# Kernel tuning notes

Hardware: AMD Instinct MI355X
Metric: run time of the kernel (lower is better)

## Reference

```python
import jax, jax.numpy as jnp
import numpy as np

EMB = 1024
HEADS = 16
HEAD_DIM = EMB // HEADS
N = 16384


def setup_inputs() -> dict:
    key = jax.random.key(0)
    ks = jax.random.split(key, 9)
    s = 1.0 / np.sqrt(EMB)
    return {
        "src": jax.random.normal(ks[0], (N, EMB), dtype=jnp.float32),
        "Wq": jax.random.normal(ks[1], (EMB, EMB), dtype=jnp.float32) * s,
        "bq": jax.random.normal(ks[2], (EMB,), dtype=jnp.float32) * s,
        "Wk": jax.random.normal(ks[3], (EMB, EMB), dtype=jnp.float32) * s,
        "bk": jax.random.normal(ks[4], (EMB,), dtype=jnp.float32) * s,
        "Wv": jax.random.normal(ks[5], (EMB, EMB), dtype=jnp.float32) * s,
        "bv": jax.random.normal(ks[6], (EMB,), dtype=jnp.float32) * s,
        "Wo": jax.random.normal(ks[7], (EMB, EMB), dtype=jnp.float32) * s,
        "bo": jax.random.normal(ks[8], (EMB,), dtype=jnp.float32) * s,
    }


def reference(src, Wq, bq, Wk, bk, Wv, bv, Wo, bo):
    # nn.Linear: y = x @ W^T + b  (W is [out, in])
    q = src @ Wq.T + bq          # [N, E]
    k = src @ Wk.T + bk
    v = src @ Wv.T + bv
    q = q.reshape(-1, HEADS, HEAD_DIM)   # [N, H, D]
    k = k.reshape(-1, HEADS, HEAD_DIM)
    v = v.reshape(-1, HEADS, HEAD_DIM)
    # NOTE: attention is across heads within each token: scores [N, H, H]
    scale = 1.0 / jnp.sqrt(jnp.float32(HEAD_DIM))
    scores = jnp.einsum('nhd,ngd->nhg', q, k) * scale   # [N, H, H]
    attn = jax.nn.softmax(scores, axis=-1)
    out = jnp.einsum('nhg,ngd->nhd', attn, v)            # [N, H, D]
    out = out.reshape(-1, EMB)
    out = out @ Wo.T + bo                                 # [N, E]
    return out.reshape(-1, HEADS, HEAD_DIM)               # [N, H, D]
```

## Files before the change

### kernel.cpp

```cpp
#include <hip/hip_runtime.h>
#include <stdint.h>
#include <stddef.h>

#define EMB 1024
#define NTOK 16384

typedef __attribute__((ext_vector_type(8))) short short8;
typedef __attribute__((ext_vector_type(4))) float floatx4;

__device__ __forceinline__ unsigned short f2bf(float f) {
    union { float f; unsigned int u; } v; v.f = f;
    unsigned int u = v.u;
    unsigned int r = (u + 0x7fffu + ((u >> 16) & 1u)) >> 16;
    return (unsigned short)r;
}
__device__ __forceinline__ float bf2f(unsigned short s) {
    union { unsigned int u; float f; } v; v.u = ((unsigned int)s) << 16;
    return v.f;
}

__device__ __forceinline__ void gload16(const void* g, void* l) {
    __builtin_amdgcn_global_load_lds(
        (const __attribute__((address_space(1))) void*)g,
        (__attribute__((address_space(3))) void*)l, 16, 0, 0);
}

__global__ void cvt_kernel(const float* __restrict__ in,
                           unsigned short* __restrict__ out, int n4) {
    int idx = blockIdx.x * blockDim.x + threadIdx.x;
    int stride = gridDim.x * blockDim.x;
    for (int i = idx; i < n4; i += stride) {
        float4 f = reinterpret_cast<const float4*>(in)[i];
        ushort4 o;
        o.x = f2bf(f.x); o.y = f2bf(f.y); o.z = f2bf(f.z); o.w = f2bf(f.w);
        reinterpret_cast<ushort4*>(out)[i] = o;
    }
}

__global__ void cvt4_kernel(const float* __restrict__ s0, const float* __restrict__ s1,
                            const float* __restrict__ s2, const float* __restrict__ s3,
                            unsigned short* __restrict__ out) {
    int idx = blockIdx.x * blockDim.x + threadIdx.x;
    const int total = 4 << 18;
    int stride = gridDim.x * blockDim.x;
    for (int i = idx; i < total; i += stride) {
        int w = i >> 18, r = i & ((1 << 18) - 1);
        const float* s = (w == 0) ? s0 : (w == 1) ? s1 : (w == 2) ? s2 : s3;
        float4 f = reinterpret_cast<const float4*>(s)[r];
        ushort4 o;
        o.x = f2bf(f.x); o.y = f2bf(f.y); o.z = f2bf(f.z); o.w = f2bf(f.w);
        reinterpret_cast<ushort4*>(out)[i] = o;
    }
}

__global__ void bias_cat_kernel(const float* __restrict__ b0,
                                const float* __restrict__ b1,
                                const float* __restrict__ b2,
                                float* __restrict__ out) {
    int i = blockIdx.x * blockDim.x + threadIdx.x;
    float v = (i < 1024) ? b0[i] : (i < 2048 ? b1[i - 1024] : b2[i - 2048]);
    out[i] = v;
}

__device__ __forceinline__ void store_val(float* C, size_t idx, float v) { C[idx] = v; }
__device__ __forceinline__ void store_val(unsigned short* C, size_t idx, float v) { C[idx] = f2bf(v); }

template<typename OUT_T>
__global__ __launch_bounds__(512, 2)
void gemm256(const unsigned short* __restrict__ A,
             const unsigned short* __restrict__ B,
             const float* __restrict__ bias,
             OUT_T* __restrict__ C,
             int K, int Nc, int grid_m)
{
    __shared__ unsigned short lds[65536];

    const int bid = blockIdx.x;
    const int cpx = gridDim.x >> 3;
    const int wg  = (bid & 7) * cpx + (bid >> 3);
    const int m0 = (wg % grid_m) * 256;
    const int n0 = (wg / grid_m) * 256;

    const int tid  = threadIdx.x;
    const int lane = tid & 63;
    const int wid  = tid >> 6;
    const int wm = (wid >> 2) * 128;
    const int wn = (wid & 3) * 64;
    const int rr = lane & 15;
    const int klo = (((lane >> 4) ^ ((rr >> 1) & 3)) << 3);

    const unsigned short* pA[2];
    const unsigned short* pB[2];
    int ldst[2];
#pragma unroll
    for (int l = 0; l < 2; ++l) {
        const int P16  = l * 512 + tid;
        const int rowS = P16 >> 2;
        const int colel = (((P16 & 3) ^ ((rowS >> 1) & 3)) << 3);
        pA[l] = A + (size_t)(m0 + rowS) * K + colel;
        pB[l] = B + (size_t)(n0 + rowS) * K + colel;
        ldst[l] = P16 * 8;
    }

    floatx4 acc[8][4];
#pragma unroll
    for (int i = 0; i < 8; ++i)
#pragma unroll
        for (int j = 0; j < 4; ++j)
            acc[i][j] = (floatx4){0.f, 0.f, 0.f, 0.f};

    const int NT = K >> 6;

#pragma unroll
    for (int l = 0; l < 2; ++l) {
        gload16(pA[l],      &lds[0     + ldst[l]]);
        gload16(pA[l] + 32, &lds[8192  + ldst[l]]);
        gload16(pB[l],      &lds[16384 + ldst[l]]);
        gload16(pB[l] + 32, &lds[24576 + ldst[l]]);
    }
    asm volatile("s_waitcnt vmcnt(0)" ::: "memory");
    asm volatile("s_barrier" ::: "memory");

    short8 afA[4], afB[4], bfA[4], bfB[4];
#pragma unroll
    for (int i = 0; i < 4; ++i)
        afA[i] = *reinterpret_cast<const short8*>(&lds[(wm + i * 16 + rr) * 32 + klo]);
#pragma unroll
    for (int j = 0; j < 4; ++j)
        bfA[j] = *reinterpret_cast<const short8*>(&lds[16384 + (wn + j * 16 + rr) * 32 + klo]);

    for (int t = 0; t < NT; ++t) {
        const int cur = (t & 1) * 32768;
        const int nxt = cur ^ 32768;
        const int ktn = (t + 1 < NT) ? (t + 1) * 64 : 0;

        gload16(pA[0] + ktn, &lds[nxt + ldst[0]]);
        gload16(pA[1] + ktn, &lds[nxt + ldst[1]]);
#pragma unroll
        for (int i = 0; i < 4; ++i)
            afB[i] = *reinterpret_cast<const short8*>(&lds[cur + (wm + 64 + i * 16 + rr) * 32 + klo]);
        asm volatile("s_barrier" ::: "memory");
        __builtin_amdgcn_s_setprio(1);
#pragma unroll
        for (int j = 0; j < 4; ++j)
#pragma unroll
            for (int i = 0; i < 4; ++i)
                acc[i][j] = __builtin_amdgcn_mfma_f32_16x16x32_bf16(afA[i], bfA[j], acc[i][j], 0, 0, 0);
        __builtin_amdgcn_s_setprio(0);
        asm volatile("s_barrier" ::: "memory");

        gload16(pB[0] + ktn, &lds[nxt + 16384 + ldst[0]]);
        gload16(pB[1] + ktn, &lds[nxt + 16384 + ldst[1]]);
        asm volatile("s_waitcnt vmcnt(4)" ::: "memory");
        asm volatile("s_barrier" ::: "memory");
#pragma unroll
        for (int i = 0; i < 4; ++i)
            afA[i] = *reinterpret_cast<const short8*>(&lds[cur + 8192 + (wm + i * 16 + rr) * 32 + klo]);
#pragma unroll
        for (int j = 0; j < 4; ++j)
            bfB[j] = *reinterpret_cast<const short8*>(&lds[cur + 24576 + (wn + j * 16 + rr) * 32 + klo]);
        __builtin_amdgcn_s_setprio(1);
#pragma unroll
        for (int j = 0; j < 4; ++j)
#pragma unroll
            for (int i = 0; i < 4; ++i)
                acc[4 + i][j] = __builtin_amdgcn_mfma_f32_16x16x32_bf16(afB[i], bfA[j], acc[4 + i][j], 0, 0, 0);
        __builtin_amdgcn_s_setprio(0);
        asm volatile("s_barrier" ::: "memory");

        gload16(pA[0] + ktn + 32, &lds[nxt + 8192 + ldst[0]]);
        gload16(pA[1] + ktn + 32, &lds[nxt + 8192 + ldst[1]]);
#pragma unroll
        for (int i = 0; i < 4; ++i)
            afB[i] = *reinterpret_cast<const short8*>(&lds[cur + 8192 + (wm + 64 + i * 16 + rr) * 32 + klo]);
        asm volatile("s_barrier" ::: "memory");
        __builtin_amdgcn_s_setprio(1);
#pragma unroll
        for (int j = 0; j < 4; ++j)
#pragma unroll
            for (int i = 0; i < 4; ++i)
                acc[i][j] = __builtin_amdgcn_mfma_f32_16x16x32_bf16(afA[i], bfB[j], acc[i][j], 0, 0, 0);
        __builtin_amdgcn_s_setprio(0);
        asm volatile("s_barrier" ::: "memory");

        gload16(pB[0] + ktn + 32, &lds[nxt + 24576 + ldst[0]]);
        gload16(pB[1] + ktn + 32, &lds[nxt + 24576 + ldst[1]]);
        asm volatile("s_waitcnt vmcnt(4)" ::: "memory");
        asm volatile("s_barrier" ::: "memory");
#pragma unroll
        for (int i = 0; i < 4; ++i)
            afA[i] = *reinterpret_cast<const short8*>(&lds[nxt + (wm + i * 16 + rr) * 32 + klo]);
#pragma unroll
        for (int j = 0; j < 4; ++j)
            bfA[j] = *reinterpret_cast<const short8*>(&lds[nxt + 16384 + (wn + j * 16 + rr) * 32 + klo]);
        __builtin_amdgcn_s_setprio(1);
#pragma unroll
        for (int j = 0; j < 4; ++j)
#pragma unroll
            for (int i = 0; i < 4; ++i)
                acc[4 + i][j] = __builtin_amdgcn_mfma_f32_16x16x32_bf16(afB[i], bfB[j], acc[4 + i][j], 0, 0, 0);
        __builtin_amdgcn_s_setprio(0);
        asm volatile("s_barrier" ::: "memory");
    }

    const int cn  = lane & 15;
    const int cm4 = (lane >> 4) * 4;
    float bv[4];
#pragma unroll
    for (int j = 0; j < 4; ++j) bv[j] = bias[n0 + wn + j * 16 + cn];
#pragma unroll
    for (int ai = 0; ai < 8; ++ai) {
        const int row = m0 + wm + (ai >> 2) * 64 + (ai & 3) * 16 + cm4;
#pragma unroll
        for (int j = 0; j < 4; ++j) {
            const int col = n0 + wn + j * 16 + cn;
#pragma unroll
            for (int r = 0; r < 4; ++r)
                store_val(C, (size_t)(row + r) * Nc + col, acc[ai][j][r] + bv[j]);
        }
    }
}

#define ROWP 72

__global__ __launch_bounds__(256)
void attn_kernel(const unsigned short* __restrict__ QKV,
                 unsigned short* __restrict__ O)
{
    const int wave = threadIdx.x >> 6;
    const int lane = threadIdx.x & 63;
    const int n = blockIdx.x * 4 + wave;

    __shared__ unsigned short lq[4][16 * ROWP];
    __shared__ unsigned short lk[4][16 * ROWP];
    __shared__ unsigned short lv[4][16 * ROWP];
    __shared__ float lp[4][256];

    {
        const unsigned short* gq = QKV + (size_t)n * 3072;
        const unsigned short* gk = gq + 1024;
        const unsigned short* gv = gq + 2048;
        for (int t = lane; t < 128; t += 64) {
            int r = t >> 3, c = t & 7;
            *reinterpret_cast<short8*>(&lq[wave][r * ROWP + c * 8]) =
                *reinterpret_cast<const short8*>(gq + t * 8);
            *reinterpret_cast<short8*>(&lk[wave][r * ROWP + c * 8]) =
                *reinterpret_cast<const short8*>(gk + t * 8);
            *reinterpret_cast<short8*>(&lv[wave][r * ROWP + c * 8]) =
                *reinterpret_cast<const short8*>(gv + t * 8);
        }
    }
    __syncthreads();

    const int g = lane & 15;
    const int a = lane >> 4;

    float kf[64];
#pragma unroll
    for (int c2 = 0; c2 < 8; ++c2) {
        short8 kv = *reinterpret_cast<const short8*>(&lk[wave][g * ROWP + c2 * 8]);
#pragma unroll
        for (int e = 0; e < 8; ++e) kf[c2 * 8 + e] = bf2f((unsigned short)kv[e]);
    }

#pragma unroll
    for (int i = 0; i < 4; ++i) {
        const int h = i * 4 + a;
        float s = 0.f;
#pragma unroll
        for (int c2 = 0; c2 < 8; ++c2) {
            short8 qv = *reinterpret_cast<const short8*>(&lq[wave][h * ROWP + c2 * 8]);
#pragma unroll
            for (int e = 0; e < 8; ++e)
                s = fmaf(bf2f((unsigned short)qv[e]), kf[c2 * 8 + e], s);
        }
        s *= 0.125f;

        float m = s;
#pragma unroll
        for (int o = 1; o < 16; o <<= 1) m = fmaxf(m, __shfl_xor(m, o, 64));
        float p = expf(s - m);
        float sum = p;
#pragma unroll
        for (int o = 1; o < 16; o <<= 1) sum += __shfl_xor(sum, o, 64);
        lp[wave][h * 16 + g] = p / sum;
    }
    __syncthreads();

    const int h = lane >> 2;
    const int db = (lane & 3) * 16;
    float o[16];
#pragma unroll
    for (int e = 0; e < 16; ++e) o[e] = 0.f;

    for (int g2 = 0; g2 < 16; ++g2) {
        const float pw = lp[wave][h * 16 + g2];
        short8 v0 = *reinterpret_cast<const short8*>(&lv[wave][g2 * ROWP + db]);
        short8 v1 = *reinterpret_cast<const short8*>(&lv[wave][g2 * ROWP + db + 8]);
#pragma unroll
        for (int e = 0; e < 8; ++e) {
            o[e]     = fmaf(pw, bf2f((unsigned short)v0[e]), o[e]);
            o[8 + e] = fmaf(pw, bf2f((unsigned short)v1[e]), o[8 + e]);
        }
    }

    short8 o0, o1;
#pragma unroll
    for (int e = 0; e < 8; ++e) {
        o0[e] = (short)f2bf(o[e]);
        o1[e] = (short)f2bf(o[8 + e]);
    }
    unsigned short* dst = O + (size_t)n * EMB + h * 64 + db;
    *reinterpret_cast<short8*>(dst) = o0;
    *reinterpret_cast<short8*>(dst + 8) = o1;
}

extern "C" void kernel_launch(void* const* d_in, const int* in_sizes, int n_in,
                              void* d_out, int out_size, void* d_ws, size_t ws_size,
                              hipStream_t stream)
{
    const float* src = (const float*)d_in[0];
    const float* Wq  = (const float*)d_in[1];
    const float* bq  = (const float*)d_in[2];
    const float* Wk  = (const float*)d_in[3];
    const float* bk  = (const float*)d_in[4];
    const float* Wv  = (const float*)d_in[5];
    const float* bv  = (const float*)d_in[6];
    const float* Wo  = (const float*)d_in[7];
    const float* bo  = (const float*)d_in[8];
    float* out = (float*)d_out;

    unsigned short* ws = (unsigned short*)d_ws;
    unsigned short* src_bf = ws;
    unsigned short* wqkv   = src_bf + (size_t)NTOK * EMB;
    unsigned short* wo_bf  = wqkv + (size_t)3 * EMB * EMB;
    unsigned short* qkv    = wo_bf + (size_t)EMB * EMB;
    unsigned short* ab     = qkv + (size_t)NTOK * 3 * EMB;
    float* bias_cat        = (float*)(ab + (size_t)NTOK * EMB);

    cvt_kernel<<<2048, 256, 0, stream>>>(src, src_bf, NTOK * EMB / 4);
    cvt4_kernel<<<2048, 256, 0, stream>>>(Wq, Wk, Wv, Wo, wqkv);
    bias_cat_kernel<<<12, 256, 0, stream>>>(bq, bk, bv, bias_cat);

    gemm256<unsigned short><<<dim3(64 * 12), 512, 0, stream>>>(
        src_bf, wqkv, bias_cat, qkv, EMB, 3 * EMB, 64);

    attn_kernel<<<NTOK / 4, 256, 0, stream>>>(qkv, ab);

    gemm256<float><<<dim3(64 * 4), 512, 0, stream>>>(
        ab, wo_bf, bo, out, EMB, EMB, 64);
}
```

Measured before the change: 227.5 us.

## Merge GEMM main-loop phases into two MFMA bursts with fewer barriers

The 256x256 bf16 GEMM inner loop is restructured from four barrier-separated MFMA phases into two phases per 64-wide K tile. Each phase issues its global-to-LDS prefetches first, then runs 32 MFMAs back to back. Per-iteration barriers drop from eight to two, and LDS fragment offsets are precomputed once per thread. The aim is to cut barrier stalls and the dependence on lockstep waves. In exchange, fragment loads overlap less with MFMA execution, and the LDS reuse ordering depends on the remaining waitcnt/barrier pairs being enough.

Measured after the change: 208.9 us. 1.09x faster.

```diff
diff --git a/kernel.cpp b/kernel.cpp
--- a/kernel.cpp
+++ b/kernel.cpp
@@ -89,6 +89,9 @@
     const int rr = lane & 15;
     const int klo = (((lane >> 4) ^ ((rr >> 1) & 3)) << 3);
 
+    const int aro = (wm + rr) * 32 + klo;
+    const int bro = 16384 + (wn + rr) * 32 + klo;
+
     const unsigned short* pA[2];
     const unsigned short* pB[2];
     int ldst[2];
@@ -121,13 +124,13 @@
     asm volatile("s_waitcnt vmcnt(0)" ::: "memory");
     asm volatile("s_barrier" ::: "memory");
 
-    short8 afA[4], afB[4], bfA[4], bfB[4];
+    short8 a0[4], a1[4], b0[4];
 #pragma unroll
     for (int i = 0; i < 4; ++i)
-        afA[i] = *reinterpret_cast<const short8*>(&lds[(wm + i * 16 + rr) * 32 + klo]);
+        a0[i] = *reinterpret_cast<const short8*>(&lds[aro + i * 512]);
 #pragma unroll
     for (int j = 0; j < 4; ++j)
-        bfA[j] = *reinterpret_cast<const short8*>(&lds[16384 + (wn + j * 16 + rr) * 32 + klo]);
+        b0[j] = *reinterpret_cast<const short8*>(&lds[bro + j * 512]);
 
     for (int t = 0; t < NT; ++t) {
         const int cur = (t & 1) * 32768;
@@ -136,71 +139,59 @@
 
         gload16(pA[0] + ktn, &lds[nxt + ldst[0]]);
         gload16(pA[1] + ktn, &lds[nxt + ldst[1]]);
-#pragma unroll
-        for (int i = 0; i < 4; ++i)
-            afB[i] = *reinterpret_cast<const short8*>(&lds[cur + (wm + 64 + i * 16 + rr) * 32 + klo]);
-        asm volatile("s_barrier" ::: "memory");
-        __builtin_amdgcn_s_setprio(1);
-#pragma unroll
-        for (int j = 0; j < 4; ++j)
-#pragma unroll
-            for (int i = 0; i < 4; ++i)
-                acc[i][j] = __builtin_amdgcn_mfma_f32_16x16x32_bf16(afA[i], bfA[j], acc[i][j], 0, 0, 0);
-        __builtin_amdgcn_s_setprio(0);
-        asm volatile("s_barrier" ::: "memory");
-
         gload16(pB[0] + ktn, &lds[nxt + 16384 + ldst[0]]);
         gload16(pB[1] + ktn, &lds[nxt + 16384 + ldst[1]]);
+#pragma unroll
+        for (int i = 0; i < 4; ++i)
+            a1[i] = *reinterpret_cast<const short8*>(&lds[cur + aro + 2048 + i * 512]);
+        __builtin_amdgcn_s_setprio(1);
+#pragma unroll
+        for (int j = 0; j < 4; ++j)
+#pragma unroll
+            for (int i = 0; i < 4; ++i)
+                acc[i][j] = __builtin_amdgcn_mfma_f32_16x16x32_bf16(a0[i], b0[j], acc[i][j], 0, 0, 0);
+#pragma unroll
+        for (int j = 0; j < 4; ++j)
+#pragma unroll
+            for (int i = 0; i < 4; ++i)
+                acc[4 + i][j] = __builtin_amdgcn_mfma_f32_16x16x32_bf16(a1[i], b0[j], acc[4 + i][j], 0, 0, 0);
+        __builtin_amdgcn_s_setprio(0);
         asm volatile("s_waitcnt vmcnt(4)" ::: "memory");
         asm volatile("s_barrier" ::: "memory");
-#pragma unroll
-        for (int i = 0; i < 4; ++i)
-            afA[i] = *reinterpret_cast<const short8*>(&lds[cur + 8192 + (wm + i * 16 + rr) * 32 + klo]);
-#pragma unroll
-        for (int j = 0; j < 4; ++j)
-            bfB[j] = *reinterpret_cast<const short8*>(&lds[cur + 24576 + (wn + j * 16 + rr) * 32 + klo]);
-        __builtin_amdgcn_s_setprio(1);
-#pragma unroll
-        for (int j = 0; j < 4; ++j)
-#pragma unroll
-            for (int i = 0; i < 4; ++i)
-                acc[4 + i][j] = __builtin_amdgcn_mfma_f32_16x16x32_bf16(afB[i], bfA[j], acc[4 + i][j], 0, 0, 0);
-        __builtin_amdgcn_s_setprio(0);
-        asm volatile("s_barrier" ::: "memory");
 
         gload16(pA[0] + ktn + 32, &lds[nxt + 8192 + ldst[0]]);
         gload16(pA[1] + ktn + 32, &lds[nxt + 8192 + ldst[1]]);
-#pragma unroll
-        for (int i = 0; i < 4; ++i)
-            afB[i] = *reinterpret_cast<const short8*>(&lds[cur + 8192 + (wm + 64 + i * 16 + rr) * 32 + klo]);
-        asm volatile("s_barrier" ::: "memory");
-        __builtin_amdgcn_s_setprio(1);
-#pragma unroll
-        for (int j = 0; j < 4; ++j)
-#pragma unroll
-            for (int i = 0; i < 4; ++i)
-                acc[i][j] = __builtin_amdgcn_mfma_f32_16x16x32_bf16(afA[i], bfB[j], acc[i][j], 0, 0, 0);
-        __builtin_amdgcn_s_setprio(0);
-        asm volatile("s_barrier" ::: "memory");
-
         gload16(pB[0] + ktn + 32, &lds[nxt + 24576 + ldst[0]]);
         gload16(pB[1] + ktn + 32, &lds[nxt + 24576 + ldst[1]]);
+#pragma unroll
+        for (int i = 0; i < 4; ++i)
+            a0[i] = *reinterpret_cast<const short8*>(&lds[cur + 8192 + aro + i * 512]);
+#pragma unroll
+        for (int j = 0; j < 4; ++j)
+            b0[j] = *reinterpret_cast<const short8*>(&lds[cur + 8192 + bro + j * 512]);
+#pragma unroll
+        for (int i = 0; i < 4; ++i)
+            a1[i] = *reinterpret_cast<const short8*>(&lds[cur + 8192 + aro + 2048 + i * 512]);
+        __builtin_amdgcn_s_setprio(1);
+#pragma unroll
+        for (int j = 0; j < 4; ++j)
+#pragma unroll
+            for (int i = 0; i < 4; ++i)
+                acc[i][j] = __builtin_amdgcn_mfma_f32_16x16x32_bf16(a0[i], b0[j], acc[i][j], 0, 0, 0);
+#pragma unroll
+        for (int j = 0; j < 4; ++j)
+#pragma unroll
+            for (int i = 0; i < 4; ++i)
+                acc[4 + i][j] = __builtin_amdgcn_mfma_f32_16x16x32_bf16(a1[i], b0[j], acc[4 + i][j], 0, 0, 0);
+        __builtin_amdgcn_s_setprio(0);
         asm volatile("s_waitcnt vmcnt(4)" ::: "memory");
         asm volatile("s_barrier" ::: "memory");
 #pragma unroll
         for (int i = 0; i < 4; ++i)
-            afA[i] = *reinterpret_cast<const short8*>(&lds[nxt + (wm + i * 16 + rr) * 32 + klo]);
-#pragma unroll
-        for (int j = 0; j < 4; ++j)
-            bfA[j] = *reinterpret_cast<const short8*>(&lds[nxt + 16384 + (wn + j * 16 + rr) * 32 + klo]);
-        __builtin_amdgcn_s_setprio(1);
-#pragma unroll
-        for (int j = 0; j < 4; ++j)
-#pragma unroll
-            for (int i = 0; i < 4; ++i)
-                acc[4 + i][j] = __builtin_amdgcn_mfma_f32_16x16x32_bf16(afB[i], bfB[j], acc[4 + i][j], 0, 0, 0);
-        __builtin_amdgcn_s_setprio(0);
-        asm volatile("s_barrier" ::: "memory");
+            a0[i] = *reinterpret_cast<const short8*>(&lds[nxt + aro + i * 512]);
+#pragma unroll
+        for (int j = 0; j < 4; ++j)
+            b0[j] = *reinterpret_cast<const short8*>(&lds[nxt + bro + j * 512]);
     }
 
     const int cn  = lane & 15;
```
